# Optimization experiments

Measured on AMD Instinct MI355X. Metric: run time of the kernel, lower is better.

## Reference

```python
import jax, jax.numpy as jnp
import numpy as np

NEG = jnp.float32(-1e30)  # filter value (stand-in for -inf, grad-safe)
EPS = 1e-5  # _SAMPLING_EPS


def setup_inputs() -> dict:
    key = jax.random.key(0)
    ks = jax.random.split(key, 6)
    B, V = 128, 128256
    logits = jax.random.normal(ks[0], (B, V), jnp.float32) * 2.0
    temperature = jax.random.uniform(ks[1], (B,), jnp.float32, 0.0, 1.5)
    min_p = jax.random.uniform(ks[2], (B,), jnp.float32, 0.0, 0.1)
    top_p = jax.random.uniform(ks[3], (B,), jnp.float32, 0.8, 0.999)
    top_k = jax.random.randint(ks[4], (B,), 1, 100).astype(jnp.int64)
    uniform_noise = jax.random.uniform(ks[5], (B, V), jnp.float32, 1e-10, 1.0)
    return dict(logits=logits, temperature=temperature, min_p=min_p,
                top_p=top_p, top_k=top_k, uniform_noise=uniform_noise,
                num_logprobs=8)


def _filter_logits(logits, temperature, min_p, top_p, top_k):
    """Sequential temperature -> min_p -> top_k -> top_p filtering, per row."""
    B, V = logits.shape
    safe_t = jnp.where(temperature < EPS, 1.0, temperature)
    x = logits / safe_t[:, None]
    # min_p: drop tokens with prob < min_p * max_prob
    probs = jax.nn.softmax(x, axis=-1)
    top_prob = probs.max(axis=-1, keepdims=True)
    x = jnp.where(probs < min_p[:, None] * top_prob, NEG, x)
    # single descending sort serves both top-k and top-p
    s = jnp.sort(x, axis=-1)[:, ::-1]  # [B, V] descending
    k = jnp.clip(top_k, 1, V).astype(jnp.int32)
    kth = jnp.take_along_axis(s, (k - 1)[:, None], axis=-1)  # k-th largest logit
    x = jnp.where(x < kth, NEG, x)
    # top-p on the top-k-masked distribution (mask doesn't reorder survivors)
    col = jnp.arange(V)[None, :]
    s_k = jnp.where(col < k[:, None], s, NEG)
    sp = jax.nn.softmax(s_k, axis=-1)
    cum = jnp.cumsum(sp, axis=-1)
    keep = (cum - sp) < top_p[:, None]  # always keeps the top token
    nkeep = jnp.maximum(keep.sum(axis=-1), 1)
    cutoff = jnp.take_along_axis(s_k, (nkeep - 1)[:, None], axis=-1)
    x = jnp.where(x < cutoff, NEG, x)
    return x


def reference(logits, temperature, min_p, top_p, top_k, uniform_noise, num_logprobs):
    logits = logits.astype(jnp.float32)
    # raw logprobs before any processing (compute_logprobs)
    raw_logprobs = jax.nn.log_softmax(logits, axis=-1)
    # greedy path
    greedy = jnp.argmax(logits, axis=-1)
    # random path: filter chain + gumbel-max categorical sampling
    x = _filter_logits(logits, temperature, min_p, top_p, top_k)
    gumbel = -jnp.log(-jnp.log(uniform_noise))
    random_sampled = jnp.argmax(x + gumbel, axis=-1)
    sampled = jnp.where(temperature < EPS, greedy, random_sampled)
    # gather_logprobs
    topk_lp, topk_idx = jax.lax.top_k(raw_logprobs, num_logprobs)
    tid = sampled[:, None]
    token_lp = jnp.take_along_axis(raw_logprobs, tid, axis=-1)  # [B,1]
    token_ranks = (raw_logprobs >= token_lp).sum(axis=-1)
    indices = jnp.concatenate([tid, topk_idx], axis=1).astype(jnp.int32)
    logprobs_out = jnp.concatenate([token_lp, topk_lp], axis=1)
    sampled_token_ids = sampled.astype(jnp.int32)[:, None]  # [B,1]
    return sampled_token_ids, indices, logprobs_out, token_ranks
```

## Files before the change

### kernel.cpp

```cpp
#include <hip/hip_runtime.h>
#include <stdint.h>
#include <math.h>

#define NS 8
#define K3B 512
#define K4B 256
#define NBINS 8192
#define SEG 320
#define CANDC 4096
#define CAND_MIN 128
#define NEGV -1e30f
#define EPSV 1e-5f

__device__ __forceinline__ uint32_t toOrd(float f) {
  uint32_t u = __float_as_uint(f);
  return (u & 0x80000000u) ? ~u : (u | 0x80000000u);
}
__device__ __forceinline__ float fromOrd(uint32_t o) {
  uint32_t u = (o & 0x80000000u) ? (o & 0x7fffffffu) : ~o;
  return __uint_as_float(u);
}

__global__ void __launch_bounds__(K3B)
k3_fused(const float* __restrict__ logits, const float* __restrict__ temp_,
         float* __restrict__ pmax, float* __restrict__ pS, float* __restrict__ pSx,
         uint32_t* __restrict__ pcnt, uint64_t* __restrict__ cand, int V)
{
  const int chunk = blockIdx.x, row = blockIdx.y;
  const int tid = threadIdx.x, lane = tid & 63, wv = tid >> 6;
  __shared__ uint32_t h[NBINS];
  __shared__ uint32_t sfx[K3B + 1];
  __shared__ float redf[8], redf2[8];
  __shared__ int s_gsel, s_bstar;
  __shared__ float s_m;
  __shared__ uint32_t s_loc;
  __shared__ uint64_t stage[SEG];

  for (int i = tid; i < NBINS; i += K3B) h[i] = 0u;
  if (tid == 0) { s_loc = 0u; s_gsel = 0; }
  __syncthreads();

  const int clen = ((V + NS - 1) / NS + 3) & ~3;
  const int start = chunk * clen;
  int valid = V - start;
  if (valid < 0) valid = 0;
  if (valid > clen) valid = clen;
  const int nf4 = valid >> 2;
  const float* crow = logits + (size_t)row * V + start;
  const float4* p4 = (const float4*)crow;

  float lmax = -INFINITY;
  for (int i = tid; i < nf4; i += K3B) {
    float4 v = p4[i];
    float a[4] = {v.x, v.y, v.z, v.w};
    #pragma unroll
    for (int c = 0; c < 4; c++) {
      lmax = fmaxf(lmax, a[c]);
      atomicAdd(&h[toOrd(a[c]) >> 19], 1u);
    }
  }
  for (int i = (nf4 << 2) + tid; i < valid; i += K3B) {
    float a = crow[i];
    lmax = fmaxf(lmax, a);
    atomicAdd(&h[toOrd(a) >> 19], 1u);
  }
  #pragma unroll
  for (int o = 32; o; o >>= 1) lmax = fmaxf(lmax, __shfl_down(lmax, o));
  if (lane == 0) redf[wv] = lmax;
  __syncthreads();

  {
    uint32_t g = 0;
    #pragma unroll
    for (int b = 0; b < 16; b++) g += h[tid * 16 + b];
    sfx[tid] = g;
    if (tid == 0) sfx[K3B] = 0;
    __syncthreads();
    for (int off = 1; off < K3B; off <<= 1) {
      uint32_t v = (tid + off < K3B) ? sfx[tid + off] : 0u;
      __syncthreads();
      sfx[tid] += v;
      __syncthreads();
    }
    uint32_t gs = sfx[tid], gn = sfx[tid + 1];
    if (gs >= CAND_MIN && gn < CAND_MIN) s_gsel = tid;
    __syncthreads();
  }
  if (tid == 0) {
    int gsl = s_gsel;
    uint32_t cum = sfx[gsl + 1];
    int bsel = gsl * 16;
    for (int b = gsl * 16 + 15; b >= gsl * 16; b--) {
      cum += h[b];
      if (cum >= CAND_MIN) { bsel = b; break; }
    }
    s_bstar = bsel;
    float mm = redf[0];
    for (int w = 1; w < 8; w++) mm = fmaxf(mm, redf[w]);
    s_m = mm;
    pmax[row * NS + chunk] = mm;
  }
  __syncthreads();

  const float m_c = s_m;
  const int bst = s_bstar;
  const float t = temp_[row];
  const float safe_t = (t < EPSV) ? 1.0f : t;
  const float m_xc = m_c / safe_t;

  float S = 0.f, Sx = 0.f;
  for (int i = tid; i < nf4; i += K3B) {
    float4 v = p4[i];
    float a[4] = {v.x, v.y, v.z, v.w};
    #pragma unroll
    for (int c = 0; c < 4; c++) {
      S += expf(a[c] - m_c);
      float x = a[c] / safe_t;
      Sx += expf(x - m_xc);
      uint32_t o = toOrd(a[c]);
      if ((int)(o >> 19) >= bst) {
        uint32_t slot = atomicAdd(&s_loc, 1u);
        if (slot < SEG)
          stage[slot] = ((uint64_t)(~o) << 32) | (uint32_t)(start + i * 4 + c);
      }
    }
  }
  for (int i = (nf4 << 2) + tid; i < valid; i += K3B) {
    float a = crow[i];
    S += expf(a - m_c);
    float x = a / safe_t;
    Sx += expf(x - m_xc);
    uint32_t o = toOrd(a);
    if ((int)(o >> 19) >= bst) {
      uint32_t slot = atomicAdd(&s_loc, 1u);
      if (slot < SEG)
        stage[slot] = ((uint64_t)(~o) << 32) | (uint32_t)(start + i);
    }
  }
  #pragma unroll
  for (int o = 32; o; o >>= 1) { S += __shfl_down(S, o); Sx += __shfl_down(Sx, o); }
  if (lane == 0) { redf[wv] = S; redf2[wv] = Sx; }
  __syncthreads();
  if (tid == 0) {
    float s = 0, sx = 0;
    for (int w = 0; w < 8; w++) { s += redf[w]; sx += redf2[w]; }
    pS[row * NS + chunk] = s;
    pSx[row * NS + chunk] = sx;
  }
  int lc = (int)s_loc; if (lc > SEG) lc = SEG;
  for (int i = tid; i < lc; i += K3B)
    cand[((size_t)row * NS + chunk) * SEG + i] = stage[i];
  if (tid == 0) pcnt[row * NS + chunk] = (uint32_t)lc;
}

__global__ void __launch_bounds__(K4B)
k4_final(const float* __restrict__ temp_, const float* __restrict__ minp_,
         const float* __restrict__ topp_, const int* __restrict__ topk_,
         const float* __restrict__ noise_,
         const float* __restrict__ pmax, const float* __restrict__ pS,
         const float* __restrict__ pSx, const uint32_t* __restrict__ pcnt,
         const uint64_t* __restrict__ candG, float* __restrict__ out,
         int B, int V, int nlp)
{
  const int row = blockIdx.x, tid = threadIdx.x, lane = tid & 63, wv = tid >> 6;
  __shared__ uint64_t cd[CANDC];
  __shared__ uint64_t cd2[CANDC];
  __shared__ uint32_t h[NBINS];
  __shared__ uint32_t sfx[K4B + 1];
  __shared__ int soff[NS + 1];
  __shared__ float redv[4], redl[4];
  __shared__ int redi[4], redr[4];
  __shared__ int s_gsel, s_bstar;
  __shared__ uint32_t s_c2;
  __shared__ float sh_kth, sh_cut, sh_mpthr, sh_m, sh_L, sh_safe_t, sh_mx, sh_Sx, sh_tlp;

  for (int i = tid; i < NBINS; i += K4B) h[i] = 0u;
  if (tid == 0) {
    int o = 0;
    for (int c = 0; c < NS; c++) {
      soff[c] = o;
      int cc = (int)pcnt[row * NS + c];
      if (cc > SEG) cc = SEG;
      o += cc;
    }
    soff[NS] = o;
    s_gsel = 0; s_c2 = 0u;
  }
  __syncthreads();
  const int total = soff[NS];
  for (int idx = tid; idx < NS * SEG; idx += K4B) {
    int c = idx / SEG, i = idx - c * SEG;
    int cc = soff[c + 1] - soff[c];
    if (i < cc) cd[soff[c] + i] = candG[((size_t)row * NS + c) * SEG + i];
  }
  __syncthreads();

  for (int e = tid; e < total; e += K4B) {
    uint32_t bin = (~(uint32_t)(cd[e] >> 32)) >> 19;
    atomicAdd(&h[bin], 1u);
  }
  __syncthreads();

  {
    uint32_t g = 0;
    #pragma unroll
    for (int b = 0; b < 32; b++) g += h[tid * 32 + b];
    sfx[tid] = g;
    if (tid == 0) sfx[K4B] = 0;
    __syncthreads();
    for (int off = 1; off < K4B; off <<= 1) {
      uint32_t v = (tid + off < K4B) ? sfx[tid + off] : 0u;
      __syncthreads();
      sfx[tid] += v;
      __syncthreads();
    }
    uint32_t gs = sfx[tid], gn = sfx[tid + 1];
    if (gs >= CAND_MIN && gn < CAND_MIN) s_gsel = tid;
    __syncthreads();
  }
  if (tid == 0) {
    int gsl = s_gsel;
    uint32_t cum = sfx[gsl + 1];
    int bsel = gsl * 32;
    for (int b = gsl * 32 + 31; b >= gsl * 32; b--) {
      cum += h[b];
      if (cum >= CAND_MIN) { bsel = b; break; }
    }
    s_bstar = bsel;
  }
  __syncthreads();

  const int bst = s_bstar;
  for (int e = tid; e < total; e += K4B) {
    uint64_t c = cd[e];
    if ((int)((~(uint32_t)(c >> 32)) >> 19) >= bst) {
      uint32_t slot = atomicAdd(&s_c2, 1u);
      cd2[slot] = c;
    }
  }
  __syncthreads();
  const int cnt2 = (int)s_c2;
  int N2 = 256; while (N2 < cnt2) N2 <<= 1;
  for (int e = cnt2 + tid; e < N2; e += K4B) cd2[e] = ~0ull;
  __syncthreads();

  for (int ks = 2; ks <= N2; ks <<= 1) {
    for (int j = ks >> 1; j; j >>= 1) {
      for (int e = tid; e < N2; e += K4B) {
        int p = e ^ j;
        if (p > e) {
          uint64_t a = cd2[e], b = cd2[p];
          bool up = ((e & ks) == 0);
          if ((a > b) == up) { cd2[e] = b; cd2[p] = a; }
        }
      }
      __syncthreads();
    }
  }

  if (tid == 0) {
    float t = temp_[row];
    float safe_t = (t < EPSV) ? 1.0f : t;
    float m = pmax[row * NS + 0];
    for (int c = 1; c < NS; c++) m = fmaxf(m, pmax[row * NS + c]);
    float m_x = m / safe_t;
    float S = 0, Sx = 0;
    for (int c = 0; c < NS; c++) {
      float mc = pmax[row * NS + c];
      S  += pS[row * NS + c]  * expf(mc - m);
      Sx += pSx[row * NS + c] * expf(mc / safe_t - m_x);
    }
    float L = logf(S);
    int i64mode = (B > 1 && topk_[1] == 0) ? 1 : 0;
    int kraw = i64mode ? topk_[2 * row] : topk_[row];
    int k = kraw < 1 ? 1 : (kraw > V ? V : kraw);
    int keff = k < cnt2 ? k : cnt2;
    float mpthr = minp_[row] * (1.0f / Sx);
    float topp = topp_[row];
    int np = 0;
    while (np < keff) {
      float xl = fromOrd(~(uint32_t)(cd2[np] >> 32)) / safe_t;
      float p = expf(xl - m_x) / Sx;
      if (p < mpthr) break;
      np++;
    }
    float kth_x = NEGV;
    if (np == k) kth_x = fromOrd(~(uint32_t)(cd2[k - 1] >> 32)) / safe_t;
    int kk = np;
    float S2 = 0.f;
    for (int i = 0; i < kk; i++)
      S2 += expf(fromOrd(~(uint32_t)(cd2[i] >> 32)) / safe_t - m_x);
    float cum = 0.f; int nkeep = 0;
    for (int i = 0; i < kk; i++) {
      float xl = fromOrd(~(uint32_t)(cd2[i] >> 32)) / safe_t;
      float sp = expf(xl - m_x) / S2;
      cum += sp;
      if (cum - sp < topp) nkeep++;
    }
    float cutoff_x = NEGV;
    if (!(cum < topp)) {
      if (nkeep < 1) nkeep = 1;
      cutoff_x = fromOrd(~(uint32_t)(cd2[nkeep - 1] >> 32)) / safe_t;
    }
    sh_kth = kth_x; sh_cut = cutoff_x; sh_mpthr = mpthr; sh_m = m; sh_L = L;
    sh_safe_t = safe_t; sh_mx = m_x; sh_Sx = Sx;
  }
  __syncthreads();

  float bestv = -INFINITY, bestl = 0.f; int besti = 0x7fffffff;
  for (int e = tid; e < cnt2; e += K4B) {
    uint64_t c = cd2[e];
    float l = fromOrd(~(uint32_t)(c >> 32));
    int idx = (int)(uint32_t)(c & 0xffffffffu);
    float x = l / sh_safe_t;
    float p = expf(x - sh_mx) / sh_Sx;
    if (p >= sh_mpthr && x >= sh_kth && x >= sh_cut) {
      float u = noise_[(size_t)row * V + idx];
      float v = x + (-logf(-logf(u)));
      if (v > bestv || (v == bestv && idx < besti)) { bestv = v; besti = idx; bestl = l; }
    }
  }
  #pragma unroll
  for (int o = 32; o; o >>= 1) {
    float ov = __shfl_down(bestv, o); int oi = __shfl_down(besti, o); float ol = __shfl_down(bestl, o);
    if (ov > bestv || (ov == bestv && oi < besti)) { bestv = ov; besti = oi; bestl = ol; }
  }
  if (lane == 0) { redv[wv] = bestv; redi[wv] = besti; redl[wv] = bestl; }
  __syncthreads();
  if (tid == 0) {
    float bv = redv[0]; int bi = redi[0]; float bl = redl[0];
    for (int w = 1; w < 4; w++) {
      if (redv[w] > bv || (redv[w] == bv && redi[w] < bi)) { bv = redv[w]; bi = redi[w]; bl = redl[w]; }
    }
    float t = temp_[row];
    int sampled; float ls;
    if (t < EPSV) {
      uint64_t c0 = cd2[0];
      sampled = (int)(uint32_t)(c0 & 0xffffffffu);
      ls = fromOrd(~(uint32_t)(c0 >> 32));
    } else { sampled = bi; ls = bl; }
    float token_lp = (ls - sh_m) - sh_L;
    sh_tlp = token_lp;
    float* out_idx = out + B;
    float* out_lp = out + B + (size_t)B * (1 + nlp);
    size_t rb = (size_t)row * (1 + nlp);
    out[row] = (float)sampled;
    out_idx[rb] = (float)sampled;
    out_lp[rb] = token_lp;
    for (int j = 0; j < nlp; j++) {
      uint64_t c = cd2[j];
      out_idx[rb + 1 + j] = (float)(int)(uint32_t)(c & 0xffffffffu);
      out_lp[rb + 1 + j] = (fromOrd(~(uint32_t)(c >> 32)) - sh_m) - sh_L;
    }
  }
  __syncthreads();

  int rc = 0;
  for (int e = tid; e < cnt2; e += K4B) {
    float l = fromOrd(~(uint32_t)(cd2[e] >> 32));
    float f = (l - sh_m) - sh_L;
    rc += (f >= sh_tlp) ? 1 : 0;
  }
  #pragma unroll
  for (int o = 32; o; o >>= 1) rc += __shfl_down(rc, o);
  if (lane == 0) redr[wv] = rc;
  __syncthreads();
  if (tid == 0) {
    int r = 0;
    for (int w = 0; w < 4; w++) r += redr[w];
    out[B + 2 * (size_t)B * (1 + nlp) + row] = (float)r;
  }
}

#define FB_BLOCK 1024
#define FB_CAP 2048
#define FB_NW 16

struct FBSM {
  uint32_t hist[NBINS];
  uint64_t cand[FB_CAP];
  float redf[FB_NW];
  int   redi[FB_NW];
  int cnt; int bstar;
  float m, S, Sx;
  float kth_x, cutoff_x, mpthr;
  float L, token_lp;
  int greedy;
};

__device__ __forceinline__ float fbCandVal(const uint64_t* cand, int i) {
  return fromOrd(~(uint32_t)(cand[i] >> 32));
}

__global__ void __launch_bounds__(FB_BLOCK)
sampler_fallback(const float* __restrict__ logits, const float* __restrict__ temp_,
                 const float* __restrict__ minp_, const float* __restrict__ topp_,
                 const int* __restrict__ topk_, const float* __restrict__ noise_,
                 float* __restrict__ out, int B, int V, int nlp)
{
  __shared__ FBSM sm;
  const int row = blockIdx.x, tid = threadIdx.x, lane = tid & 63, wv = tid >> 6;
  const float* lrow = logits + (size_t)row * V;
  const float* nrow = noise_ + (size_t)row * V;
  const int V4 = V >> 2, Vt = V4 << 2;
  const float4* l4 = (const float4*)lrow;
  const float4* n4 = (const float4*)nrow;
  for (int i = tid; i < NBINS; i += FB_BLOCK) sm.hist[i] = 0u;
  if (tid == 0) sm.cnt = 0;
  __syncthreads();
  float lmax = -INFINITY;
  for (int i = tid; i < V4; i += FB_BLOCK) {
    float4 v = l4[i]; float a[4] = {v.x, v.y, v.z, v.w};
    #pragma unroll
    for (int c = 0; c < 4; c++) { lmax = fmaxf(lmax, a[c]); atomicAdd(&sm.hist[toOrd(a[c]) >> 19], 1u); }
  }
  for (int i = Vt + tid; i < V; i += FB_BLOCK) {
    float a = lrow[i]; lmax = fmaxf(lmax, a); atomicAdd(&sm.hist[toOrd(a) >> 19], 1u);
  }
  #pragma unroll
  for (int o = 32; o; o >>= 1) lmax = fmaxf(lmax, __shfl_down(lmax, o));
  if (lane == 0) sm.redf[wv] = lmax;
  __syncthreads();
  if (tid == 0) {
    float mm = sm.redf[0];
    for (int w = 1; w < FB_NW; w++) mm = fmaxf(mm, sm.redf[w]);
    sm.m = mm;
    uint32_t cum = 0; int b = NBINS - 1;
    for (; b > 0; b--) { cum += sm.hist[b]; if (cum >= CAND_MIN) break; }
    sm.bstar = b;
  }
  __syncthreads();
  const float m = sm.m;
  const int bstar = sm.bstar;
  const float t = temp_[row];
  const float safe_t = (t < EPSV) ? 1.0f : t;
  const float m_x = m / safe_t;
  float S = 0.f, Sx = 0.f;
  for (int i = tid; i < V4; i += FB_BLOCK) {
    float4 v = l4[i]; float a[4] = {v.x, v.y, v.z, v.w};
    #pragma unroll
    for (int c = 0; c < 4; c++) {
      S += expf(a[c] - m);
      float x = a[c] / safe_t; Sx += expf(x - m_x);
      uint32_t o = toOrd(a[c]);
      if ((int)(o >> 19) >= bstar) {
        int slot = atomicAdd(&sm.cnt, 1);
        if (slot < FB_CAP) sm.cand[slot] = ((uint64_t)(~o) << 32) | (uint32_t)(i * 4 + c);
      }
    }
  }
  for (int i = Vt + tid; i < V; i += FB_BLOCK) {
    float a = lrow[i];
    S += expf(a - m);
    float x = a / safe_t; Sx += expf(x - m_x);
    uint32_t o = toOrd(a);
    if ((int)(o >> 19) >= bstar) {
      int slot = atomicAdd(&sm.cnt, 1);
      if (slot < FB_CAP) sm.cand[slot] = ((uint64_t)(~o) << 32) | (uint32_t)i;
    }
  }
  #pragma unroll
  for (int o = 32; o; o >>= 1) { S += __shfl_down(S, o); Sx += __shfl_down(Sx, o); }
  if (lane == 0) sm.redf[wv] = S;
  __syncthreads();
  if (tid == 0) { float s = 0; for (int w = 0; w < FB_NW; w++) s += sm.redf[w]; sm.S = s; }
  __syncthreads();
  if (lane == 0) sm.redf[wv] = Sx;
  __syncthreads();
  if (tid == 0) { float s = 0; for (int w = 0; w < FB_NW; w++) s += sm.redf[w]; sm.Sx = s; }
  __syncthreads();
  const int count = min(sm.cnt, FB_CAP);
  for (int i = count + tid; i < FB_CAP; i += FB_BLOCK) sm.cand[i] = ~0ull;
  __syncthreads();
  for (int ks = 2; ks <= FB_CAP; ks <<= 1) {
    for (int j = ks >> 1; j > 0; j >>= 1) {
      for (int e = tid; e < FB_CAP; e += FB_BLOCK) {
        int p = e ^ j;
        if (p > e) {
          uint64_t a = sm.cand[e], b2 = sm.cand[p];
          bool up = ((e & ks) == 0);
          if ((a > b2) == up) { sm.cand[e] = b2; sm.cand[p] = a; }
        }
      }
      __syncthreads();
    }
  }
  if (tid == 0) {
    const float Sx_ = sm.Sx;
    const float L = logf(sm.S);
    sm.L = L;
    int i64mode = (B > 1 && topk_[1] == 0) ? 1 : 0;
    int kraw = i64mode ? topk_[2 * row] : topk_[row];
    int k = kraw < 1 ? 1 : (kraw > V ? V : kraw);
    int keff = k < count ? k : count;
    float mpthr = minp_[row] * (1.0f / Sx_);
    sm.mpthr = mpthr;
    float topp = topp_[row];
    int np = 0;
    while (np < keff) {
      float xl = fbCandVal(sm.cand, np) / safe_t;
      float p = expf(xl - m_x) / Sx_;
      if (p < mpthr) break;
      np++;
    }
    float kth_x = NEGV;
    if (np == k) kth_x = fbCandVal(sm.cand, k - 1) / safe_t;
    int kk = np;
    float S2 = 0.f;
    for (int i = 0; i < kk; i++) S2 += expf(fbCandVal(sm.cand, i) / safe_t - m_x);
    float cum = 0.f; int nkeep = 0;
    for (int i = 0; i < kk; i++) {
      float xl = fbCandVal(sm.cand, i) / safe_t;
      float sp = expf(xl - m_x) / S2;
      cum += sp;
      if (cum - sp < topp) nkeep++;
    }
    float cutoff_x = NEGV;
    if (!(cum < topp)) { if (nkeep < 1) nkeep = 1; cutoff_x = fbCandVal(sm.cand, nkeep - 1) / safe_t; }
    sm.kth_x = kth_x; sm.cutoff_x = cutoff_x;
    sm.greedy = (int)(uint32_t)(sm.cand[0] & 0xffffffffu);
  }
  __syncthreads();
  const float kth_x = sm.kth_x, cutoff_x = sm.cutoff_x, mpthr = sm.mpthr, SxR = sm.Sx;
  float bestv = -INFINITY; int besti = 0;
  for (int i = tid; i < V4; i += FB_BLOCK) {
    float4 lv = l4[i]; float4 uv = n4[i];
    float la[4] = {lv.x, lv.y, lv.z, lv.w};
    float ua[4] = {uv.x, uv.y, uv.z, uv.w};
    #pragma unroll
    for (int c = 0; c < 4; c++) {
      float x = la[c] / safe_t;
      float p = expf(x - m_x) / SxR;
      float val = NEGV;
      if (p >= mpthr && x >= kth_x && x >= cutoff_x) val = x + (-logf(-logf(ua[c])));
      if (val > bestv) { bestv = val; besti = i * 4 + c; }
    }
  }
  for (int i = Vt + tid; i < V; i += FB_BLOCK) {
    float x = lrow[i] / safe_t;
    float p = expf(x - m_x) / SxR;
    float val = NEGV;
    if (p >= mpthr && x >= kth_x && x >= cutoff_x) val = x + (-logf(-logf(nrow[i])));
    if (val > bestv) { bestv = val; besti = i; }
  }
  #pragma unroll
  for (int o = 32; o; o >>= 1) {
    float ov = __shfl_down(bestv, o); int oi = __shfl_down(besti, o);
    if (ov > bestv || (ov == bestv && oi < besti)) { bestv = ov; besti = oi; }
  }
  if (lane == 0) { sm.redf[wv] = bestv; sm.redi[wv] = besti; }
  __syncthreads();
  if (tid == 0) {
    float bv = sm.redf[0]; int bi = sm.redi[0];
    for (int w = 1; w < FB_NW; w++) {
      if (sm.redf[w] > bv || (sm.redf[w] == bv && sm.redi[w] < bi)) { bv = sm.redf[w]; bi = sm.redi[w]; }
    }
    int sampled = (t < EPSV) ? sm.greedy : bi;
    float ls = lrow[sampled];
    float token_lp = (ls - m) - sm.L;
    sm.token_lp = token_lp;
    float* out_idx = out + B;
    float* out_lp = out + B + (size_t)B * (1 + nlp);
    size_t rb = (size_t)row * (1 + nlp);
    out[row] = (float)sampled;
    out_idx[rb] = (float)sampled;
    out_lp[rb] = token_lp;
    for (int j = 0; j < nlp; j++) {
      uint64_t cdv = sm.cand[j];
      out_idx[rb + 1 + j] = (float)(int)(uint32_t)(cdv & 0xffffffffu);
      out_lp[rb + 1 + j] = (fromOrd(~(uint32_t)(cdv >> 32)) - m) - sm.L;
    }
  }
  __syncthreads();
  const float Lc = sm.L, tlp = sm.token_lp;
  int cnt = 0;
  for (int i = tid; i < V4; i += FB_BLOCK) {
    float4 v = l4[i]; float a[4] = {v.x, v.y, v.z, v.w};
    #pragma unroll
    for (int c = 0; c < 4; c++) { float lp = (a[c] - m) - Lc; cnt += (lp >= tlp) ? 1 : 0; }
  }
  for (int i = Vt + tid; i < V; i += FB_BLOCK) {
    float lp = (lrow[i] - m) - Lc; cnt += (lp >= tlp) ? 1 : 0;
  }
  #pragma unroll
  for (int o = 32; o; o >>= 1) cnt += __shfl_down(cnt, o);
  if (lane == 0) sm.redi[wv] = cnt;
  __syncthreads();
  if (tid == 0) {
    int r = 0;
    for (int w = 0; w < FB_NW; w++) r += sm.redi[w];
    out[B + 2 * (size_t)B * (1 + nlp) + row] = (float)r;
  }
}

extern "C" void kernel_launch(void* const* d_in, const int* in_sizes, int n_in,
                              void* d_out, int out_size, void* d_ws, size_t ws_size,
                              hipStream_t stream) {
  const float* logits = (const float*)d_in[0];
  const float* temp   = (const float*)d_in[1];
  const float* minp   = (const float*)d_in[2];
  const float* topp   = (const float*)d_in[3];
  const int*   topk   = (const int*)d_in[4];
  const float* noise  = (const float*)d_in[5];
  int B = in_sizes[1];
  int V = in_sizes[0] / B;
  int nlp = (out_size / B - 4) / 2;
  if (nlp < 0) nlp = 0;

  uint8_t* ws = (uint8_t*)d_ws;
  size_t off = 0;
  uint32_t* pcnt = (uint32_t*)(ws + off); off += (size_t)B * NS * 4;
  float* pmax = (float*)(ws + off); off += (size_t)B * NS * 4;
  float* pS   = (float*)(ws + off); off += (size_t)B * NS * 4;
  float* pSx  = (float*)(ws + off); off += (size_t)B * NS * 4;
  off = (off + 7) & ~(size_t)7;
  uint64_t* cand = (uint64_t*)(ws + off); off += (size_t)B * NS * SEG * 8;

  if (ws_size < off) {
    hipLaunchKernelGGL(sampler_fallback, dim3(B), dim3(FB_BLOCK), 0, stream,
                       logits, temp, minp, topp, topk, noise, (float*)d_out, B, V, nlp);
    return;
  }

  hipLaunchKernelGGL(k3_fused, dim3(NS, B), dim3(K3B), 0, stream,
                     logits, temp, pmax, pS, pSx, pcnt, cand, V);
  hipLaunchKernelGGL(k4_final, dim3(B), dim3(K4B), 0, stream,
                     temp, minp, topp, topk, noise, pmax, pS, pSx, pcnt, cand,
                     (float*)d_out, B, V, nlp);
}
```

Measured before the change: 222.4 us.

## Drop temperature-softmax sum by rewriting min_p test as exp ratio

The min_p test is rewritten algebraically as exp(x - max_x) >= min_p. The probability ratio to the top probability does not depend on the temperature-scaled normaliser, so k3 no longer computes the second exp and divide per element, or the Sx partial sums. The shared-memory suffix scan in k3 is replaced with a wave-shuffle scan plus per-wave totals, which removes many barriers. In k4, the scaled logits and their exponentials are precomputed in parallel into shared arrays, so the serial thread-0 loops and the sampling loop reuse them instead of recomputing. The k4 shared arrays use a union to limit LDS growth, at a small precision risk at the min_p threshold boundary.

Measured after the change: 184.3 us. 17.2% less time.

```diff
diff --git a/kernel.cpp b/kernel.cpp
--- a/kernel.cpp
+++ b/kernel.cpp
@@ -22,15 +22,16 @@
 }
 
 __global__ void __launch_bounds__(K3B)
-k3_fused(const float* __restrict__ logits, const float* __restrict__ temp_,
-         float* __restrict__ pmax, float* __restrict__ pS, float* __restrict__ pSx,
+k3_fused(const float* __restrict__ logits,
+         float* __restrict__ pmax, float* __restrict__ pS,
          uint32_t* __restrict__ pcnt, uint64_t* __restrict__ cand, int V)
 {
   const int chunk = blockIdx.x, row = blockIdx.y;
   const int tid = threadIdx.x, lane = tid & 63, wv = tid >> 6;
   __shared__ uint32_t h[NBINS];
-  __shared__ uint32_t sfx[K3B + 1];
-  __shared__ float redf[8], redf2[8];
+  __shared__ uint32_t sfx[K3B];
+  __shared__ uint32_t wtot[8];
+  __shared__ float redf[8];
   __shared__ int s_gsel, s_bstar;
   __shared__ float s_m;
   __shared__ uint32_t s_loc;
@@ -73,22 +74,27 @@
     uint32_t g = 0;
     #pragma unroll
     for (int b = 0; b < 16; b++) g += h[tid * 16 + b];
-    sfx[tid] = g;
-    if (tid == 0) sfx[K3B] = 0;
+    uint32_t x = g;
+    #pragma unroll
+    for (int off = 1; off < 64; off <<= 1) {
+      uint32_t v = __shfl_down(x, off);
+      if (lane + off < 64) x += v;
+    }
+    if (lane == 0) wtot[wv] = x;
     __syncthreads();
-    for (int off = 1; off < K3B; off <<= 1) {
-      uint32_t v = (tid + off < K3B) ? sfx[tid + off] : 0u;
-      __syncthreads();
-      sfx[tid] += v;
-      __syncthreads();
-    }
-    uint32_t gs = sfx[tid], gn = sfx[tid + 1];
+    uint32_t tail = 0;
+    for (int w = wv + 1; w < 8; w++) tail += wtot[w];
+    uint32_t gs = x + tail;
+    uint32_t gn = gs - g;
+    sfx[tid] = gs;
     if (gs >= CAND_MIN && gn < CAND_MIN) s_gsel = tid;
     __syncthreads();
   }
   if (tid == 0) {
     int gsl = s_gsel;
-    uint32_t cum = sfx[gsl + 1];
+    uint32_t gg = 0;
+    for (int b = 0; b < 16; b++) gg += h[gsl * 16 + b];
+    uint32_t cum = sfx[gsl] - gg;
     int bsel = gsl * 16;
     for (int b = gsl * 16 + 15; b >= gsl * 16; b--) {
       cum += h[b];
@@ -104,19 +110,14 @@
 
   const float m_c = s_m;
   const int bst = s_bstar;
-  const float t = temp_[row];
-  const float safe_t = (t < EPSV) ? 1.0f : t;
-  const float m_xc = m_c / safe_t;
-
-  float S = 0.f, Sx = 0.f;
+
+  float S = 0.f;
   for (int i = tid; i < nf4; i += K3B) {
     float4 v = p4[i];
     float a[4] = {v.x, v.y, v.z, v.w};
     #pragma unroll
     for (int c = 0; c < 4; c++) {
       S += expf(a[c] - m_c);
-      float x = a[c] / safe_t;
-      Sx += expf(x - m_xc);
       uint32_t o = toOrd(a[c]);
       if ((int)(o >> 19) >= bst) {
         uint32_t slot = atomicAdd(&s_loc, 1u);
@@ -128,8 +129,6 @@
   for (int i = (nf4 << 2) + tid; i < valid; i += K3B) {
     float a = crow[i];
     S += expf(a - m_c);
-    float x = a / safe_t;
-    Sx += expf(x - m_xc);
     uint32_t o = toOrd(a);
     if ((int)(o >> 19) >= bst) {
       uint32_t slot = atomicAdd(&s_loc, 1u);
@@ -138,14 +137,13 @@
     }
   }
   #pragma unroll
-  for (int o = 32; o; o >>= 1) { S += __shfl_down(S, o); Sx += __shfl_down(Sx, o); }
-  if (lane == 0) { redf[wv] = S; redf2[wv] = Sx; }
-  __syncthreads();
-  if (tid == 0) {
-    float s = 0, sx = 0;
-    for (int w = 0; w < 8; w++) { s += redf[w]; sx += redf2[w]; }
+  for (int o = 32; o; o >>= 1) S += __shfl_down(S, o);
+  if (lane == 0) redf[wv] = S;
+  __syncthreads();
+  if (tid == 0) {
+    float s = 0;
+    for (int w = 0; w < 8; w++) s += redf[w];
     pS[row * NS + chunk] = s;
-    pSx[row * NS + chunk] = sx;
   }
   int lc = (int)s_loc; if (lc > SEG) lc = SEG;
   for (int i = tid; i < lc; i += K3B)
@@ -153,17 +151,23 @@
   if (tid == 0) pcnt[row * NS + chunk] = (uint32_t)lc;
 }
 
+union K4U {
+  uint64_t cd[CANDC];
+  struct { float xl[CANDC]; } px;
+};
+
 __global__ void __launch_bounds__(K4B)
 k4_final(const float* __restrict__ temp_, const float* __restrict__ minp_,
          const float* __restrict__ topp_, const int* __restrict__ topk_,
          const float* __restrict__ noise_,
          const float* __restrict__ pmax, const float* __restrict__ pS,
-         const float* __restrict__ pSx, const uint32_t* __restrict__ pcnt,
+         const uint32_t* __restrict__ pcnt,
          const uint64_t* __restrict__ candG, float* __restrict__ out,
          int B, int V, int nlp)
 {
   const int row = blockIdx.x, tid = threadIdx.x, lane = tid & 63, wv = tid >> 6;
-  __shared__ uint64_t cd[CANDC];
+  __shared__ K4U u;
+  __shared__ float exA[CANDC];
   __shared__ uint64_t cd2[CANDC];
   __shared__ uint32_t h[NBINS];
   __shared__ uint32_t sfx[K4B + 1];
@@ -172,7 +176,7 @@
   __shared__ int redi[4], redr[4];
   __shared__ int s_gsel, s_bstar;
   __shared__ uint32_t s_c2;
-  __shared__ float sh_kth, sh_cut, sh_mpthr, sh_m, sh_L, sh_safe_t, sh_mx, sh_Sx, sh_tlp;
+  __shared__ float sh_kth, sh_cut, sh_mpthr, sh_m, sh_L, sh_safe_t, sh_mx, sh_tlp;
 
   for (int i = tid; i < NBINS; i += K4B) h[i] = 0u;
   if (tid == 0) {
@@ -191,12 +195,12 @@
   for (int idx = tid; idx < NS * SEG; idx += K4B) {
     int c = idx / SEG, i = idx - c * SEG;
     int cc = soff[c + 1] - soff[c];
-    if (i < cc) cd[soff[c] + i] = candG[((size_t)row * NS + c) * SEG + i];
+    if (i < cc) u.cd[soff[c] + i] = candG[((size_t)row * NS + c) * SEG + i];
   }
   __syncthreads();
 
   for (int e = tid; e < total; e += K4B) {
-    uint32_t bin = (~(uint32_t)(cd[e] >> 32)) >> 19;
+    uint32_t bin = (~(uint32_t)(u.cd[e] >> 32)) >> 19;
     atomicAdd(&h[bin], 1u);
   }
   __syncthreads();
@@ -232,7 +236,7 @@
 
   const int bst = s_bstar;
   for (int e = tid; e < total; e += K4B) {
-    uint64_t c = cd[e];
+    uint64_t c = u.cd[e];
     if ((int)((~(uint32_t)(c >> 32)) >> 19) >= bst) {
       uint32_t slot = atomicAdd(&s_c2, 1u);
       cd2[slot] = c;
@@ -258,66 +262,71 @@
     }
   }
 
+  int k_ = 0, keff_ = 0; float topp_v = 0.f;
   if (tid == 0) {
     float t = temp_[row];
     float safe_t = (t < EPSV) ? 1.0f : t;
     float m = pmax[row * NS + 0];
     for (int c = 1; c < NS; c++) m = fmaxf(m, pmax[row * NS + c]);
-    float m_x = m / safe_t;
-    float S = 0, Sx = 0;
-    for (int c = 0; c < NS; c++) {
-      float mc = pmax[row * NS + c];
-      S  += pS[row * NS + c]  * expf(mc - m);
-      Sx += pSx[row * NS + c] * expf(mc / safe_t - m_x);
-    }
+    float S = 0;
+    for (int c = 0; c < NS; c++) S += pS[row * NS + c] * expf(pmax[row * NS + c] - m);
     float L = logf(S);
     int i64mode = (B > 1 && topk_[1] == 0) ? 1 : 0;
     int kraw = i64mode ? topk_[2 * row] : topk_[row];
     int k = kraw < 1 ? 1 : (kraw > V ? V : kraw);
-    int keff = k < cnt2 ? k : cnt2;
-    float mpthr = minp_[row] * (1.0f / Sx);
-    float topp = topp_[row];
+    k_ = k; keff_ = k < cnt2 ? k : cnt2;
+    topp_v = topp_[row];
+    sh_m = m; sh_L = L; sh_safe_t = safe_t; sh_mx = m / safe_t;
+    sh_mpthr = minp_[row];
+  }
+  __syncthreads();
+
+  {
+    const float st = sh_safe_t, mx = sh_mx;
+    for (int e = tid; e < cnt2; e += K4B) {
+      float xl = fromOrd(~(uint32_t)(cd2[e] >> 32)) / st;
+      u.px.xl[e] = xl;
+      exA[e] = expf(xl - mx);
+    }
+  }
+  __syncthreads();
+
+  if (tid == 0) {
+    const float mpthr = sh_mpthr;
     int np = 0;
-    while (np < keff) {
-      float xl = fromOrd(~(uint32_t)(cd2[np] >> 32)) / safe_t;
-      float p = expf(xl - m_x) / Sx;
-      if (p < mpthr) break;
-      np++;
-    }
+    while (np < keff_ && exA[np] >= mpthr) np++;
     float kth_x = NEGV;
-    if (np == k) kth_x = fromOrd(~(uint32_t)(cd2[k - 1] >> 32)) / safe_t;
+    if (np == k_) kth_x = u.px.xl[k_ - 1];
     int kk = np;
     float S2 = 0.f;
-    for (int i = 0; i < kk; i++)
-      S2 += expf(fromOrd(~(uint32_t)(cd2[i] >> 32)) / safe_t - m_x);
+    for (int i = 0; i < kk; i++) S2 += exA[i];
     float cum = 0.f; int nkeep = 0;
     for (int i = 0; i < kk; i++) {
-      float xl = fromOrd(~(uint32_t)(cd2[i] >> 32)) / safe_t;
-      float sp = expf(xl - m_x) / S2;
+      float sp = exA[i] / S2;
       cum += sp;
-      if (cum - sp < topp) nkeep++;
+      if (cum - sp < topp_v) nkeep++;
     }
     float cutoff_x = NEGV;
-    if (!(cum < topp)) {
+    if (!(cum < topp_v)) {
       if (nkeep < 1) nkeep = 1;
-      cutoff_x = fromOrd(~(uint32_t)(cd2[nkeep - 1] >> 32)) / safe_t;
-    }
-    sh_kth = kth_x; sh_cut = cutoff_x; sh_mpthr = mpthr; sh_m = m; sh_L = L;
-    sh_safe_t = safe_t; sh_mx = m_x; sh_Sx = Sx;
-  }
-  __syncthreads();
-
+      cutoff_x = u.px.xl[nkeep - 1];
+    }
+    sh_kth = kth_x; sh_cut = cutoff_x;
+  }
+  __syncthreads();
+
+  const float kth = sh_kth, cut = sh_cut, mpthr = sh_mpthr;
   float bestv = -INFINITY, bestl = 0.f; int besti = 0x7fffffff;
   for (int e = tid; e < cnt2; e += K4B) {
-    uint64_t c = cd2[e];
-    float l = fromOrd(~(uint32_t)(c >> 32));
-    int idx = (int)(uint32_t)(c & 0xffffffffu);
-    float x = l / sh_safe_t;
-    float p = expf(x - sh_mx) / sh_Sx;
-    if (p >= sh_mpthr && x >= sh_kth && x >= sh_cut) {
-      float u = noise_[(size_t)row * V + idx];
-      float v = x + (-logf(-logf(u)));
-      if (v > bestv || (v == bestv && idx < besti)) { bestv = v; besti = idx; bestl = l; }
+    float xl = u.px.xl[e];
+    if (exA[e] >= mpthr && xl >= kth && xl >= cut) {
+      uint64_t c = cd2[e];
+      int idx = (int)(uint32_t)(c & 0xffffffffu);
+      float un = noise_[(size_t)row * V + idx];
+      float v = xl + (-logf(-logf(un)));
+      if (v > bestv || (v == bestv && idx < besti)) {
+        bestv = v; besti = idx; bestl = fromOrd(~(uint32_t)(c >> 32));
+      }
     }
   }
   #pragma unroll
@@ -612,7 +621,6 @@
   uint32_t* pcnt = (uint32_t*)(ws + off); off += (size_t)B * NS * 4;
   float* pmax = (float*)(ws + off); off += (size_t)B * NS * 4;
   float* pS   = (float*)(ws + off); off += (size_t)B * NS * 4;
-  float* pSx  = (float*)(ws + off); off += (size_t)B * NS * 4;
   off = (off + 7) & ~(size_t)7;
   uint64_t* cand = (uint64_t*)(ws + off); off += (size_t)B * NS * SEG * 8;
 
@@ -623,8 +631,8 @@
   }
 
   hipLaunchKernelGGL(k3_fused, dim3(NS, B), dim3(K3B), 0, stream,
-                     logits, temp, pmax, pS, pSx, pcnt, cand, V);
+                     logits, pmax, pS, pcnt, cand, V);
   hipLaunchKernelGGL(k4_final, dim3(B), dim3(K4B), 0, stream,
-                     temp, minp, topp, topk, noise, pmax, pS, pSx, pcnt, cand,
+                     temp, minp, topp, topk, noise, pmax, pS, pcnt, cand,
                      (float*)d_out, B, V, nlp);
 }
```
